# Optimization experiments

Measured on AMD Instinct MI355X. Metric: run time of the kernel, lower is better.

## Reference

```python
import jax, jax.numpy as jnp
import numpy as np

S, B, H = 2048, 4, 2048
NH = 16
HD = H // NH


def setup_inputs() -> dict:
    key = jax.random.key(0)
    ks = jax.random.split(key, 12)
    sc = 0.02
    return {
        "x": jax.random.normal(ks[0], (S, B, H), dtype=jnp.float32),
        "ln1_g": jnp.ones((H,), jnp.float32),
        "ln1_b": jnp.zeros((H,), jnp.float32),
        "qkv_w": jax.random.normal(ks[1], (3 * H, H), jnp.float32) * sc,
        "qkv_b": jnp.zeros((3 * H,), jnp.float32),
        "proj_w": jax.random.normal(ks[2], (H, H), jnp.float32) * sc,
        "proj_b": jnp.zeros((H,), jnp.float32),
        "ln2_g": jnp.ones((H,), jnp.float32),
        "ln2_b": jnp.zeros((H,), jnp.float32),
        "fc1_w": jax.random.normal(ks[3], (4 * H, H), jnp.float32) * sc,
        "fc1_b": jnp.zeros((4 * H,), jnp.float32),
        "fc2_w": jax.random.normal(ks[4], (H, 4 * H), jnp.float32) * sc,
        "fc2_b": jnp.zeros((H,), jnp.float32),
    }


def _layernorm(x, g, b, eps=1e-5):
    mu = jnp.mean(x, axis=-1, keepdims=True)
    var = jnp.mean((x - mu) ** 2, axis=-1, keepdims=True)
    return (x - mu) * jax.lax.rsqrt(var + eps) * g + b


def reference(x, ln1_g, ln1_b, qkv_w, qkv_b, proj_w, proj_b,
              ln2_g, ln2_b, fc1_w, fc1_b, fc2_w, fc2_b):
    # x: [S, B, H] (seq-first, as in original). Dropout is identity (eval mode).
    residual = x
    h = _layernorm(x, ln1_g, ln1_b)
    qkv = h @ qkv_w.T + qkv_b                       # [S, B, 3H]
    qkv = qkv.reshape(S, B, 3, NH, HD)
    q = jnp.transpose(qkv[:, :, 0], (1, 2, 0, 3))   # [B, NH, S, HD]
    k = jnp.transpose(qkv[:, :, 1], (1, 2, 0, 3))
    v = jnp.transpose(qkv[:, :, 2], (1, 2, 0, 3))
    scores = jnp.einsum("bhsd,bhtd->bhst", q, k) / jnp.sqrt(jnp.float32(HD))
    causal = jnp.tril(jnp.ones((S, S), dtype=bool))
    scores = jnp.where(causal, scores, jnp.float32(-jnp.inf))
    attn = jax.nn.softmax(scores, axis=-1)
    out = jnp.einsum("bhst,bhtd->bhsd", attn, v)    # [B, NH, S, HD]
    out = jnp.transpose(out, (2, 0, 1, 3)).reshape(S, B, H)
    out = out @ proj_w.T + proj_b
    x = residual + out
    residual = x
    h = _layernorm(x, ln2_g, ln2_b)
    h = h @ fc1_w.T + fc1_b
    h = jax.nn.gelu(h, approximate=False)
    h = h @ fc2_w.T + fc2_b
    return residual + h
```

## Files before the change

kernel.cpp:

```cpp
#include <hip/hip_runtime.h>
#include <hip/hip_bf16.h>
#include <cstdint>
#include <cstddef>

#define TOK 8192
#define HDIM 2048
#define H3 6144

typedef float f32x4 __attribute__((ext_vector_type(4)));
typedef short bf16x8 __attribute__((ext_vector_type(8)));
typedef int   i32x4 __attribute__((ext_vector_type(4)));
typedef unsigned short u16;
typedef unsigned int u32;
typedef u32 u32x2 __attribute__((ext_vector_type(2)));
typedef u32 u32x4 __attribute__((ext_vector_type(4)));

#define SLN  28.222222f
#define SW   1058.3333f
#define DQ   3.3480095e-5f

__device__ __forceinline__ u16 f2bf(float f) {
  union { float f; u32 u; } v; v.f = f;
  u32 u = v.u;
  return (u16)((u + 0x7fffu + ((u >> 16) & 1u)) >> 16);
}

__device__ __forceinline__ int q8(float v, float s) {
  int q = (int)rintf(v * s);
  return q < -127 ? -127 : (q > 127 ? 127 : q);
}

__device__ __forceinline__ float gelu_fast(float v) {
  const float u = 0.7978845608028654f * (v + 0.044715f * v * v * v);
  const float t = 1.0f - 2.0f / (__expf(2.0f * u) + 1.0f);
  return 0.5f * v * (1.0f + t);
}

__device__ __forceinline__ void gload16(const void* g, void* l) {
  __builtin_amdgcn_global_load_lds((const __attribute__((address_space(1))) u32*)g,
                                   (__attribute__((address_space(3))) u32*)l, 16, 0, 0);
}

#define GBAR()   __builtin_amdgcn_s_barrier()
#define GLGK0()  asm volatile("s_waitcnt lgkmcnt(0)" ::: "memory")
#define GVM(n)   asm volatile("s_waitcnt vmcnt(" #n ")" ::: "memory")
#define SCHED0() __builtin_amdgcn_sched_barrier(0)

__global__ __launch_bounds__(256)
void cvt_kernel(const float* __restrict__ in, u16* __restrict__ out, int n4) {
  int i = blockIdx.x * 256 + threadIdx.x;
  if (i >= n4) return;
  float4 v = ((const float4*)in)[i];
  union { u16 o[4]; u32x2 d; } t;
  t.o[0] = f2bf(v.x); t.o[1] = f2bf(v.y); t.o[2] = f2bf(v.z); t.o[3] = f2bf(v.w);
  ((u32x2*)out)[i] = t.d;
}

__global__ __launch_bounds__(256)
void cvt_i8_kernel(const float* __restrict__ in, char* __restrict__ out, int n4) {
  int i = blockIdx.x * 256 + threadIdx.x;
  if (i >= n4) return;
  float4 v = ((const float4*)in)[i];
  union { char c[4]; u32 d; } t;
  t.c[0] = (char)q8(v.x, SW); t.c[1] = (char)q8(v.y, SW);
  t.c[2] = (char)q8(v.z, SW); t.c[3] = (char)q8(v.w, SW);
  ((u32*)out)[i] = t.d;
}

template <int I8>
__global__ __launch_bounds__(256)
void ln_kernel(const float* __restrict__ x, const float* __restrict__ g,
               const float* __restrict__ bta, u16* __restrict__ out) {
  const int row = blockIdx.x, tid = threadIdx.x;
  const int lane = tid & 63, w = tid >> 6;
  const float* xr = x + (size_t)row * HDIM + tid * 8;
  float4 a = *(const float4*)xr;
  float4 c = *(const float4*)(xr + 4);
  float s = a.x + a.y + a.z + a.w + c.x + c.y + c.z + c.w;
  float q = a.x*a.x + a.y*a.y + a.z*a.z + a.w*a.w + c.x*c.x + c.y*c.y + c.z*c.z + c.w*c.w;
#pragma unroll
  for (int m = 32; m >= 1; m >>= 1) { s += __shfl_xor(s, m, 64); q += __shfl_xor(q, m, 64); }
  __shared__ float red[8];
  if (lane == 0) { red[w] = s; red[4 + w] = q; }
  __syncthreads();
  s = red[0] + red[1] + red[2] + red[3];
  q = red[4] + red[5] + red[6] + red[7];
  const float mu = s * (1.0f / HDIM);
  const float rstd = rsqrtf(q * (1.0f / HDIM) - mu * mu + 1e-5f);
  const float* gp = g + tid * 8; const float* bp = bta + tid * 8;
  float4 g0 = *(const float4*)gp, g1 = *(const float4*)(gp + 4);
  float4 b0 = *(const float4*)bp, b1 = *(const float4*)(bp + 4);
  float v[8];
  v[0] = (a.x - mu) * rstd * g0.x + b0.x;
  v[1] = (a.y - mu) * rstd * g0.y + b0.y;
  v[2] = (a.z - mu) * rstd * g0.z + b0.z;
  v[3] = (a.w - mu) * rstd * g0.w + b0.w;
  v[4] = (c.x - mu) * rstd * g1.x + b1.x;
  v[5] = (c.y - mu) * rstd * g1.y + b1.y;
  v[6] = (c.z - mu) * rstd * g1.z + b1.z;
  v[7] = (c.w - mu) * rstd * g1.w + b1.w;
  if constexpr (I8) {
    union { char c8[8]; u32x2 d; } t;
#pragma unroll
    for (int j = 0; j < 8; ++j) t.c8[j] = (char)q8(v[j], SLN);
    *(u32x2*)((char*)out + (size_t)row * HDIM + tid * 8) = t.d;
  } else {
    union { u16 o[8]; u32x4 d; } t;
#pragma unroll
    for (int j = 0; j < 8; ++j) t.o[j] = f2bf(v[j]);
    *(u32x4*)(out + (size_t)row * HDIM + tid * 8) = t.d;
  }
}

template <int EPI>
__global__ __launch_bounds__(256, 2)
void gemm128(const u16* __restrict__ A, const u16* __restrict__ Bm,
             const float* __restrict__ bias, const float* __restrict__ resid,
             u16* __restrict__ Cb, float* __restrict__ Cf, int M, int N, int K) {
  __shared__ u16 lds[16384];
  char* Lb = (char*)lds;
  const int tid = threadIdx.x;
  const int lane = tid & 63, w = tid >> 6;
  const int wr = w >> 1, wc = w & 1;
  const int l15 = lane & 15, hi = lane >> 4;

  const int tm = blockIdx.y * 128, tn = blockIdx.x * 128;

  const size_t rsK = (size_t)K * 2;
  const int scb = ((lane & 3) ^ ((lane >> 3) & 3)) * 16;
  const char* gA = (const char*)A + (size_t)(tm + w * 32 + (lane >> 2)) * rsK + scb;
  const char* gB = (const char*)Bm + (size_t)(tn + w * 32 + (lane >> 2)) * rsK + scb;
  char* sA = Lb + w * 2048;
  char* sB = Lb + 8192 + w * 2048;

#define STG(tt) do {                                                \
    const int _bo = ((tt) & 1) * 16384;                             \
    const size_t _ko = (size_t)(tt) * 64;                           \
    gload16(gA + _ko, sA + _bo);                                    \
    gload16(gA + _ko + (size_t)16 * rsK, sA + _bo + 1024);          \
    gload16(gB + _ko, sB + _bo);                                    \
    gload16(gB + _ko + (size_t)16 * rsK, sB + _bo + 1024);          \
  } while (0)

  f32x4 acc[4][4] = {};
  const int fo = (hi ^ ((l15 >> 1) & 3)) * 16;

  const int NT = K >> 5;
  STG(0);

  for (int t = 0; t < NT; ++t) {
    if (t + 1 < NT) { STG(t + 1); GVM(4); } else { GVM(0); }
    GBAR();

    const char* sb = Lb + (t & 1) * 16384;
    bf16x8 af[4], bfr[4];
#pragma unroll
    for (int i = 0; i < 4; ++i) {
      af[i]  = *(const bf16x8*)(sb + (wr * 64 + i * 16 + l15) * 64 + fo);
      bfr[i] = *(const bf16x8*)(sb + 8192 + (wc * 64 + i * 16 + l15) * 64 + fo);
    }
    __builtin_amdgcn_s_setprio(1);
#pragma unroll
    for (int mi = 0; mi < 4; ++mi)
#pragma unroll
      for (int ni = 0; ni < 4; ++ni)
        acc[mi][ni] = __builtin_amdgcn_mfma_f32_16x16x32_bf16(af[mi], bfr[ni], acc[mi][ni], 0, 0, 0);
    __builtin_amdgcn_s_setprio(0);
    GLGK0();
    GBAR();
  }

  const int colbase = tn + wc * 64 + l15;
  const int rowbase = tm + wr * 64 + hi * 4;
#pragma unroll
  for (int mi = 0; mi < 4; ++mi) {
#pragma unroll
    for (int ni = 0; ni < 4; ++ni) {
      const int col = colbase + ni * 16;
      const float bv = bias[col];
#pragma unroll
      for (int r = 0; r < 4; ++r) {
        const int row = rowbase + mi * 16 + r;
        float v = acc[mi][ni][r] + bv;
        if constexpr (EPI == 1) v = gelu_fast(v);
        const size_t idx = (size_t)row * N + col;
        if constexpr (EPI == 2) Cf[idx] = v + resid[idx];
        else                    Cb[idx] = f2bf(v);
      }
    }
  }
#undef STG
}

__global__ __launch_bounds__(256, 2)
void gemm128_i8(const char* __restrict__ A, const char* __restrict__ Bm,
                const float* __restrict__ bias, u16* __restrict__ Cb,
                int M, int N, int K) {
  __shared__ u16 lds[16384];
  char* Lb = (char*)lds;
  const int tid = threadIdx.x;
  const int lane = tid & 63, w = tid >> 6;
  const int wr = w >> 1, wc = w & 1;
  const int l15 = lane & 15, hi = lane >> 4;

  const int tm = blockIdx.y * 128, tn = blockIdx.x * 128;

  const size_t rsK = (size_t)K;
  const int scb = ((lane & 3) ^ ((lane >> 3) & 3)) * 16;
  const char* gA = A + (size_t)(tm + w * 32 + (lane >> 2)) * rsK + scb;
  const char* gB = Bm + (size_t)(tn + w * 32 + (lane >> 2)) * rsK + scb;
  char* sA = Lb + w * 2048;
  char* sB = Lb + 8192 + w * 2048;

#define STG(tt) do {                                                \
    const int _bo = ((tt) & 1) * 16384;                             \
    const size_t _ko = (size_t)(tt) * 64;                           \
    gload16(gA + _ko, sA + _bo);                                    \
    gload16(gA + _ko + (size_t)16 * rsK, sA + _bo + 1024);          \
    gload16(gB + _ko, sB + _bo);                                    \
    gload16(gB + _ko + (size_t)16 * rsK, sB + _bo + 1024);          \
  } while (0)

  i32x4 acc[4][4] = {};
  const int fo = (hi ^ ((l15 >> 1) & 3)) * 16;

  const int NT = K >> 6;
  STG(0);

  for (int t = 0; t < NT; ++t) {
    if (t + 1 < NT) { STG(t + 1); GVM(4); } else { GVM(0); }
    GBAR();

    const char* sb = Lb + (t & 1) * 16384;
    i32x4 af[4], bfr[4];
#pragma unroll
    for (int i = 0; i < 4; ++i) {
      af[i]  = *(const i32x4*)(sb + (wr * 64 + i * 16 + l15) * 64 + fo);
      bfr[i] = *(const i32x4*)(sb + 8192 + (wc * 64 + i * 16 + l15) * 64 + fo);
    }
    __builtin_amdgcn_s_setprio(1);
#pragma unroll
    for (int mi = 0; mi < 4; ++mi)
#pragma unroll
      for (int ni = 0; ni < 4; ++ni)
        acc[mi][ni] = __builtin_amdgcn_mfma_i32_16x16x64_i8(af[mi], bfr[ni], acc[mi][ni], 0, 0, 0);
    __builtin_amdgcn_s_setprio(0);
    GLGK0();
    GBAR();
  }

  const int colbase = tn + wc * 64 + l15;
  const int rowbase = tm + wr * 64 + hi * 4;
#pragma unroll
  for (int mi = 0; mi < 4; ++mi) {
#pragma unroll
    for (int ni = 0; ni < 4; ++ni) {
      const int col = colbase + ni * 16;
      const float bv = bias[col];
#pragma unroll
      for (int r = 0; r < 4; ++r) {
        const int row = rowbase + mi * 16 + r;
        float v = (float)acc[mi][ni][r] * DQ + bv;
        v = gelu_fast(v);
        Cb[(size_t)row * N + col] = f2bf(v);
      }
    }
  }
#undef STG
}

template <int EPI>
__global__ __launch_bounds__(512, 1)
void gemm256(const u16* __restrict__ A, const u16* __restrict__ Bm,
             const float* __restrict__ bias, const float* __restrict__ resid,
             u16* __restrict__ Cb, float* __restrict__ Cf, int M, int N, int K) {
  __shared__ u16 lds[65536];
  char* Lb = (char*)lds;
  const int tid = threadIdx.x;
  const int lane = tid & 63, w = tid >> 6;
  const int wm = w >> 2, wn = w & 3;
  const int l15 = lane & 15, hi = lane >> 4;

  const int gx = gridDim.x;
  const int nwg = gx * gridDim.y;
  int wgid = blockIdx.y * gx + blockIdx.x;
  wgid = (wgid & 7) * (nwg >> 3) + (wgid >> 3);
  const int tm = (wgid / gx) * 256, tn = (wgid % gx) * 256;

  const size_t rsK = (size_t)K * 2;
  const int srow8 = tid >> 3;
  const int scb   = ((tid & 7) ^ ((tid >> 3) & 7)) * 16;
  const char* gA = (const char*)A + (size_t)(tm + srow8) * rsK + scb;
  const char* gB = (const char*)Bm + (size_t)(tn + srow8) * rsK + scb;

#define STGH(o, h, tt) do {                                                    \
    char* _d = Lb + ((((tt) & 1) << 16) + (o) * 32768 + (h) * 16384 + tid * 16); \
    const char* _s = (o) ? gB : gA;                                            \
    const size_t _off = (size_t)(tt) * 128 + (size_t)((h) * 128) * rsK;        \
    gload16(_s + _off, _d);                                                    \
    gload16(_s + _off + (size_t)64 * rsK, _d + 8192);                          \
  } while (0)

  int koff[2];
#pragma unroll
  for (int ks = 0; ks < 2; ++ks) koff[ks] = ((ks * 4 + hi) ^ (l15 & 7)) * 16;

#define LDA(qm, dst) do {                                                      \
    _Pragma("unroll")                                                          \
    for (int mi4 = 0; mi4 < 4; ++mi4)                                          \
      _Pragma("unroll")                                                        \
      for (int ks = 0; ks < 2; ++ks)                                           \
        dst[mi4][ks] = *(const bf16x8*)(Lb + bb + wm * 16384 +                 \
            ((qm) * 64 + mi4 * 16 + l15) * 128 + koff[ks]);                    \
  } while (0)

#define LDB(qn) do {                                                           \
    _Pragma("unroll")                                                          \
    for (int ni = 0; ni < 2; ++ni)                                             \
      _Pragma("unroll")                                                        \
      for (int ks = 0; ks < 2; ++ks)                                           \
        bf[ni][ks] = *(const bf16x8*)(Lb + bb + 32768 + (wn >> 1) * 16384 +    \
            ((wn & 1) * 64 + (qn) * 32 + ni * 16 + l15) * 128 + koff[ks]);     \
  } while (0)

#define MFMA16(qm, qn, src) do {                                               \
    __builtin_amdgcn_s_setprio(1);                                             \
    _Pragma("unroll")                                                          \
    for (int ks = 0; ks < 2; ++ks)                                             \
      _Pragma("unroll")                                                        \
      for (int mi4 = 0; mi4 < 4; ++mi4)                                        \
        _Pragma("unroll")                                                      \
        for (int ni = 0; ni < 2; ++ni)                                         \
          acc[(qm) * 4 + mi4][(qn) * 2 + ni] =                                 \
            __builtin_amdgcn_mfma_f32_16x16x32_bf16(src[mi4][ks], bf[ni][ks],  \
                acc[(qm) * 4 + mi4][(qn) * 2 + ni], 0, 0, 0);                  \
    __builtin_amdgcn_s_setprio(0);                                             \
  } while (0)

  f32x4 acc[8][4] = {};
  bf16x8 af0[4][2], af1[4][2], bf[2][2];

  const int NT = K >> 6;

  STGH(0, 0, 0); STGH(0, 1, 0); STGH(1, 0, 0); STGH(1, 1, 0);
  STGH(0, 0, 1); STGH(0, 1, 1);
  SCHED0(); GVM(4); GBAR();

  for (int t = 0; t < NT; ++t) {
    const int bb = (t & 1) << 16;
    const bool sB = (t + 1 < NT), sA = (t + 2 < NT);
    LDA(0, af0); LDB(0);
    if (sB) STGH(1, 0, t + 1);
    SCHED0(); GBAR(); GLGK0(); SCHED0(); MFMA16(0, 0, af0); GBAR();
    LDA(1, af1);
    if (sB) STGH(1, 1, t + 1);
    SCHED0(); GBAR(); GLGK0(); SCHED0(); MFMA16(1, 0, af1); GBAR();
    LDB(1);
    if (sA) STGH(0, 0, t + 2);
    SCHED0(); GBAR(); GLGK0(); SCHED0(); MFMA16(0, 1, af0); GBAR();
    if (sA) STGH(0, 1, t + 2);
    SCHED0(); MFMA16(1, 1, af1);
    if (sA) GVM(4); else GVM(0);
    GBAR();
  }

#pragma unroll
  for (int mi = 0; mi < 8; ++mi) {
#pragma unroll
    for (int ni = 0; ni < 4; ++ni) {
      const int col = tn + wn * 64 + ni * 16 + l15;
      const float bv = bias[col];
#pragma unroll
      for (int r = 0; r < 4; ++r) {
        const int row = tm + wm * 128 + mi * 16 + hi * 4 + r;
        float v = acc[mi][ni][r] + bv;
        if constexpr (EPI == 1) v = gelu_fast(v);
        const size_t idx = (size_t)row * N + col;
        if constexpr (EPI == 2) Cf[idx] = v + resid[idx];
        else                    Cb[idx] = f2bf(v);
      }
    }
  }
#undef STGH
#undef LDA
#undef LDB
#undef MFMA16
}

__global__ __launch_bounds__(256)
void vtrans_kernel(const u16* __restrict__ qkv, u16* __restrict__ vt) {
  __shared__ u16 tile[32 * 136];
  const int s0 = blockIdx.x * 32;
  const int bh = blockIdx.y;
  const int b = bh >> 4, h = bh & 15;
  const int t = threadIdx.x;
  const int srow = t >> 3, scol = (t & 7) * 16;
  const u16* src = qkv + (size_t)((s0 + srow) * 4 + b) * H3 + 4096 + h * 128 + scol;
  *(bf16x8*)(tile + srow * 136 + scol)     = *(const bf16x8*)src;
  *(bf16x8*)(tile + srow * 136 + scol + 8) = *(const bf16x8*)(src + 8);
  __syncthreads();
  const int d = t >> 1, sc = (t & 1) * 16;
  union { u16 o[16]; u32x4 q[2]; } tmp;
#pragma unroll
  for (int i = 0; i < 16; ++i) tmp.o[i] = tile[(sc + i) * 136 + d];
  u16* dst = vt + ((size_t)bh * 128 + d) * 2048 + s0 + sc;
  *(u32x4*)dst       = tmp.q[0];
  *(u32x4*)(dst + 8) = tmp.q[1];
}

__global__ __launch_bounds__(256, 2)
void attn_kernel(const u16* __restrict__ qkv, const u16* __restrict__ vt,
                 u16* __restrict__ outb) {
  const int qt = 31 - blockIdx.x;
  const int bh = blockIdx.y;
  const int b = bh >> 4, h = bh & 15;
  const int tid = threadIdx.x, lane = tid & 63, w = tid >> 6;
  const int hi = lane >> 4, l15 = lane & 15;
  const int qs = qt * 64;

  __shared__ u16 Klds[64 * 128];
  __shared__ u16 Vlds[128 * 64];
  __shared__ u16 Plds[4 * 16 * 64];

  bf16x8 qf[4];
  {
    const int qrow = qs + w * 16 + l15;
    const u16* qp = qkv + (size_t)(qrow * 4 + b) * H3 + h * 128 + hi * 8;
#pragma unroll
    for (int kc = 0; kc < 4; ++kc) qf[kc] = *(const bf16x8*)(qp + kc * 32);
  }

  f32x4 o[8] = {};
  float mrun = -1e30f, lrun = 0.0f;

  const float sc = 0.08838834764831845f;
  char* plb = (char*)(Plds + w * 1024);

  const int krow = tid >> 2;
  const int kcb  = (tid & 3) * 64;
  const int vd   = tid >> 1;
  const int vhb  = (tid & 1) * 64;

  const int ntiles = qt + 1;
  for (int kt = 0; kt < ntiles; ++kt) {
    const int kv0 = kt * 64;
    const u16* ksrc = qkv + (size_t)((kv0 + krow) * 4 + b) * H3 + 2048 + h * 128 + kcb / 2;
    const u16* vsrc = vt + ((size_t)bh * 128 + vd) * 2048 + kv0 + (tid & 1) * 32;
    bf16x8 kr[4], vr[4];
#pragma unroll
    for (int c = 0; c < 4; ++c) { kr[c] = *(const bf16x8*)(ksrc + c * 8); vr[c] = *(const bf16x8*)(vsrc + c * 8); }

    __syncthreads();
#pragma unroll
    for (int c = 0; c < 4; ++c) {
      *(bf16x8*)((char*)Klds + ((krow * 256 + kcb + c * 16) ^ ((krow & 7) << 4))) = kr[c];
      *(bf16x8*)((char*)Vlds + ((vd * 128 + vhb + c * 16) ^ ((vd & 7) << 4)))     = vr[c];
    }
    __syncthreads();

    f32x4 s[4] = {};
#pragma unroll
    for (int kc = 0; kc < 4; ++kc) {
      const int dbyte = kc * 64 + hi * 16;
#pragma unroll
      for (int g = 0; g < 4; ++g) {
        const int row = g * 16 + l15;
        bf16x8 kf = *(const bf16x8*)((char*)Klds + ((row * 256 + dbyte) ^ ((l15 & 7) << 4)));
        s[g] = __builtin_amdgcn_mfma_f32_16x16x32_bf16(kf, qf[kc], s[g], 0, 0, 0);
      }
    }
#pragma unroll
    for (int g = 0; g < 4; ++g)
#pragma unroll
      for (int r = 0; r < 4; ++r) s[g][r] *= sc;

    if (kt == qt) {
      const int qrel = w * 16 + l15;
#pragma unroll
      for (int g = 0; g < 4; ++g)
#pragma unroll
        for (int r = 0; r < 4; ++r)
          if (g * 16 + hi * 4 + r > qrel) s[g][r] = -1e30f;
    }

    float pm = s[0][0];
#pragma unroll
    for (int g = 0; g < 4; ++g)
#pragma unroll
      for (int r = 0; r < 4; ++r) pm = fmaxf(pm, s[g][r]);
    pm = fmaxf(pm, __shfl_xor(pm, 16, 64));
    pm = fmaxf(pm, __shfl_xor(pm, 32, 64));

    const float mnew = fmaxf(mrun, pm);
    const bool need = mnew > mrun;
    const float corr = __expf(mrun - mnew);
    mrun = mnew;

    float p[4][4];
    float rs = 0.0f;
#pragma unroll
    for (int g = 0; g < 4; ++g)
#pragma unroll
      for (int r = 0; r < 4; ++r) { p[g][r] = __expf(s[g][r] - mnew); rs += p[g][r]; }
    rs += __shfl_xor(rs, 16, 64);
    rs += __shfl_xor(rs, 32, 64);
    lrun = lrun * corr + rs;

    if (__any(need)) {
      float corrq[4];
#pragma unroll
      for (int r = 0; r < 4; ++r) corrq[r] = __shfl(corr, hi * 4 + r, 64);
#pragma unroll
      for (int nf = 0; nf < 8; ++nf)
#pragma unroll
        for (int r = 0; r < 4; ++r) o[nf][r] *= corrq[r];
    }

#pragma unroll
    for (int g = 0; g < 4; ++g) {
      union { u16 h4[4]; u32x2 d; } pk;
#pragma unroll
      for (int r = 0; r < 4; ++r) pk.h4[r] = f2bf(p[g][r]);
      *(u32x2*)(plb + ((l15 * 128 + g * 32 + hi * 8) ^ ((l15 & 7) << 4))) = pk.d;
    }
    asm volatile("s_waitcnt lgkmcnt(0)" ::: "memory");
    bf16x8 pf[2];
#pragma unroll
    for (int hk = 0; hk < 2; ++hk)
      pf[hk] = *(const bf16x8*)(plb + ((l15 * 128 + hk * 64 + hi * 16) ^ ((l15 & 7) << 4)));

#pragma unroll
    for (int hk = 0; hk < 2; ++hk)
#pragma unroll
      for (int nf = 0; nf < 8; ++nf) {
        bf16x8 vf = *(const bf16x8*)((char*)Vlds +
                      (((nf * 16 + l15) * 128 + hk * 64 + hi * 16) ^ ((l15 & 7) << 4)));
        o[nf] = __builtin_amdgcn_mfma_f32_16x16x32_bf16(pf[hk], vf, o[nf], 0, 0, 0);
      }
  }

  const float inv = 1.0f / lrun;
  float invq[4];
#pragma unroll
  for (int r = 0; r < 4; ++r) invq[r] = __shfl(inv, hi * 4 + r, 64);
#pragma unroll
  for (int nf = 0; nf < 8; ++nf) {
#pragma unroll
    for (int r = 0; r < 4; ++r) {
      const int rl = hi * 4 + r;
      const int t = (qs + w * 16 + rl) * 4 + b;
      outb[(size_t)t * HDIM + h * 128 + nf * 16 + l15] = f2bf(o[nf][r] * invq[r]);
    }
  }
}

extern "C" void kernel_launch(void* const* d_in, const int* in_sizes, int n_in,
                              void* d_out, int out_size, void* d_ws, size_t ws_size,
                              hipStream_t stream) {
  const float* x     = (const float*)d_in[0];
  const float* ln1g  = (const float*)d_in[1];
  const float* ln1b  = (const float*)d_in[2];
  const float* qkvw  = (const float*)d_in[3];
  const float* qkvb  = (const float*)d_in[4];
  const float* projw = (const float*)d_in[5];
  const float* projb = (const float*)d_in[6];
  const float* ln2g  = (const float*)d_in[7];
  const float* ln2b  = (const float*)d_in[8];
  const float* fc1w  = (const float*)d_in[9];
  const float* fc1b  = (const float*)d_in[10];
  const float* fc2w  = (const float*)d_in[11];
  const float* fc2b  = (const float*)d_in[12];
  float* out = (float*)d_out;

  u16* wbuf = (u16*)d_ws;
  u16* pbuf = (u16*)((char*)d_ws + (size_t)32 * 1024 * 1024);
  u16* qbuf = (u16*)((char*)d_ws + (size_t)64 * 1024 * 1024);
  u16* vtg  = (u16*)d_ws;
  u16* aout = (u16*)((char*)d_ws + (size_t)160 * 1024 * 1024);

  dim3 blk(256);
  dim3 gblk(512);

  ln_kernel<0><<<8192, blk, 0, stream>>>(x, ln1g, ln1b, pbuf);
  cvt_kernel<<<12288, blk, 0, stream>>>(qkvw, wbuf, 3145728);
  gemm256<0><<<dim3(24, 32), gblk, 0, stream>>>(pbuf, wbuf, qkvb, nullptr, qbuf, nullptr, 8192, 6144, 2048);
  vtrans_kernel<<<dim3(64, 64), blk, 0, stream>>>(qbuf, vtg);
  attn_kernel<<<dim3(32, 64), blk, 0, stream>>>(qbuf, vtg, aout);
  cvt_kernel<<<4096, blk, 0, stream>>>(projw, wbuf, 1048576);
  gemm128<2><<<dim3(16, 64), blk, 0, stream>>>(aout, wbuf, projb, x, nullptr, out, 8192, 2048, 2048);
  ln_kernel<1><<<8192, blk, 0, stream>>>(out, ln2g, ln2b, pbuf);
  cvt_i8_kernel<<<16384, blk, 0, stream>>>(fc1w, (char*)wbuf, 4194304);
  gemm128_i8<<<dim3(64, 64), blk, 0, stream>>>((const char*)pbuf, (const char*)wbuf, fc1b, qbuf, 8192, 8192, 2048);
  cvt_kernel<<<16384, blk, 0, stream>>>(fc2w, wbuf, 4194304);
  gemm256<2><<<dim3(8, 32), gblk, 0, stream>>>(qbuf, wbuf, fc2b, out, nullptr, out, 8192, 2048, 8192);
}
```

Before: 1.033 ms.

## Double-buffer K/V tiles in LDS with two-ahead register prefetch in attention

The attention kernel now keeps two LDS buffers for K and V. It prefetches tile kt+2 into registers while computing tile kt, and writes tile kt+1 into the other buffer during the current tile's QK phase. This replaces two barriers per tile with one and overlaps global loads with MFMA and softmax work. The cost is twice the K/V LDS footprint (about 72KB per block with launch_bounds 256,2) and extra register pressure from holding two prefetch register sets, either of which may reduce occupancy or cause spills.

```diff
diff --git a/kernel.cpp b/kernel.cpp
--- a/kernel.cpp
+++ b/kernel.cpp
@@ -418,8 +418,8 @@
   const int hi = lane >> 4, l15 = lane & 15;
   const int qs = qt * 64;
 
-  __shared__ u16 Klds[64 * 128];
-  __shared__ u16 Vlds[128 * 64];
+  __shared__ u16 Klds[2][64 * 128];
+  __shared__ u16 Vlds[2][128 * 64];
   __shared__ u16 Plds[4 * 16 * 64];
 
   bf16x8 qf[4];
@@ -434,7 +434,7 @@
   float mrun = -1e30f, lrun = 0.0f;
 
   const float sc = 0.08838834764831845f;
-  char* plb = (char*)(Plds + w * 1024);
+  char* plb = (char*)Plds + w * 2048;
 
   const int krow = tid >> 2;
   const int kcb  = (tid & 3) * 64;
@@ -442,102 +442,120 @@
   const int vhb  = (tid & 1) * 64;
 
   const int ntiles = qt + 1;
-  for (int kt = 0; kt < ntiles; ++kt) {
-    const int kv0 = kt * 64;
-    const u16* ksrc = qkv + (size_t)((kv0 + krow) * 4 + b) * H3 + 2048 + h * 128 + kcb / 2;
-    const u16* vsrc = vt + ((size_t)bh * 128 + vd) * 2048 + kv0 + (tid & 1) * 32;
-    bf16x8 kr[4], vr[4];
-#pragma unroll
-    for (int c = 0; c < 4; ++c) { kr[c] = *(const bf16x8*)(ksrc + c * 8); vr[c] = *(const bf16x8*)(vsrc + c * 8); }
-
-    __syncthreads();
-#pragma unroll
-    for (int c = 0; c < 4; ++c) {
-      *(bf16x8*)((char*)Klds + ((krow * 256 + kcb + c * 16) ^ ((krow & 7) << 4))) = kr[c];
-      *(bf16x8*)((char*)Vlds + ((vd * 128 + vhb + c * 16) ^ ((vd & 7) << 4)))     = vr[c];
-    }
-    __syncthreads();
-
-    f32x4 s[4] = {};
-#pragma unroll
-    for (int kc = 0; kc < 4; ++kc) {
-      const int dbyte = kc * 64 + hi * 16;
-#pragma unroll
-      for (int g = 0; g < 4; ++g) {
-        const int row = g * 16 + l15;
-        bf16x8 kf = *(const bf16x8*)((char*)Klds + ((row * 256 + dbyte) ^ ((l15 & 7) << 4)));
-        s[g] = __builtin_amdgcn_mfma_f32_16x16x32_bf16(kf, qf[kc], s[g], 0, 0, 0);
-      }
-    }
-#pragma unroll
-    for (int g = 0; g < 4; ++g)
-#pragma unroll
-      for (int r = 0; r < 4; ++r) s[g][r] *= sc;
-
-    if (kt == qt) {
-      const int qrel = w * 16 + l15;
-#pragma unroll
-      for (int g = 0; g < 4; ++g)
-#pragma unroll
-        for (int r = 0; r < 4; ++r)
-          if (g * 16 + hi * 4 + r > qrel) s[g][r] = -1e30f;
-    }
-
-    float pm = s[0][0];
-#pragma unroll
-    for (int g = 0; g < 4; ++g)
-#pragma unroll
-      for (int r = 0; r < 4; ++r) pm = fmaxf(pm, s[g][r]);
-    pm = fmaxf(pm, __shfl_xor(pm, 16, 64));
-    pm = fmaxf(pm, __shfl_xor(pm, 32, 64));
-
-    const float mnew = fmaxf(mrun, pm);
-    const bool need = mnew > mrun;
-    const float corr = __expf(mrun - mnew);
-    mrun = mnew;
-
-    float p[4][4];
-    float rs = 0.0f;
-#pragma unroll
-    for (int g = 0; g < 4; ++g)
-#pragma unroll
-      for (int r = 0; r < 4; ++r) { p[g][r] = __expf(s[g][r] - mnew); rs += p[g][r]; }
-    rs += __shfl_xor(rs, 16, 64);
-    rs += __shfl_xor(rs, 32, 64);
-    lrun = lrun * corr + rs;
-
-    if (__any(need)) {
-      float corrq[4];
-#pragma unroll
-      for (int r = 0; r < 4; ++r) corrq[r] = __shfl(corr, hi * 4 + r, 64);
-#pragma unroll
-      for (int nf = 0; nf < 8; ++nf)
-#pragma unroll
-        for (int r = 0; r < 4; ++r) o[nf][r] *= corrq[r];
-    }
-
-#pragma unroll
-    for (int g = 0; g < 4; ++g) {
-      union { u16 h4[4]; u32x2 d; } pk;
-#pragma unroll
-      for (int r = 0; r < 4; ++r) pk.h4[r] = f2bf(p[g][r]);
-      *(u32x2*)(plb + ((l15 * 128 + g * 32 + hi * 8) ^ ((l15 & 7) << 4))) = pk.d;
-    }
-    asm volatile("s_waitcnt lgkmcnt(0)" ::: "memory");
-    bf16x8 pf[2];
-#pragma unroll
-    for (int hk = 0; hk < 2; ++hk)
-      pf[hk] = *(const bf16x8*)(plb + ((l15 * 128 + hk * 64 + hi * 16) ^ ((l15 & 7) << 4)));
-
-#pragma unroll
-    for (int hk = 0; hk < 2; ++hk)
-#pragma unroll
-      for (int nf = 0; nf < 8; ++nf) {
-        bf16x8 vf = *(const bf16x8*)((char*)Vlds +
-                      (((nf * 16 + l15) * 128 + hk * 64 + hi * 16) ^ ((l15 & 7) << 4)));
-        o[nf] = __builtin_amdgcn_mfma_f32_16x16x32_bf16(pf[hk], vf, o[nf], 0, 0, 0);
-      }
-  }
+
+  bf16x8 krA[4], vrA[4], krB[4], vrB[4];
+
+#define LOADT(tt, kr, vr) do {                                                  \
+    const u16* ks_ = qkv + (size_t)(((tt) * 64 + krow) * 4 + b) * H3 + 2048 + h * 128 + kcb / 2; \
+    const u16* vs_ = vt + ((size_t)bh * 128 + vd) * 2048 + (tt) * 64 + (tid & 1) * 32; \
+    _Pragma("unroll")                                                           \
+    for (int c = 0; c < 4; ++c) { kr[c] = *(const bf16x8*)(ks_ + c * 8);        \
+                                  vr[c] = *(const bf16x8*)(vs_ + c * 8); }      \
+  } while (0)
+
+#define WRITET(bb, kr, vr) do {                                                 \
+    _Pragma("unroll")                                                           \
+    for (int c = 0; c < 4; ++c) {                                               \
+      *(bf16x8*)((char*)Klds[bb] + ((krow * 256 + kcb + c * 16) ^ ((krow & 7) << 4))) = kr[c]; \
+      *(bf16x8*)((char*)Vlds[bb] + ((vd * 128 + vhb + c * 16) ^ ((vd & 7) << 4)))     = vr[c]; \
+    }                                                                           \
+  } while (0)
+
+#define TILE_BODY(CUR, KRN, VRN, KRL, VRL) do {                                 \
+              \
+    f32x4 s[4] = {};                                                            \
+    _Pragma("unroll")                                                           \
+    for (int kc = 0; kc < 4; ++kc) {                                            \
+      const int dbyte = kc * 64 + hi * 16;                                      \
+      _Pragma("unroll")                                                         \
+      for (int g = 0; g < 4; ++g) {                                             \
+        const int row = g * 16 + l15;                                           \
+        bf16x8 kf = *(const bf16x8*)((char*)Klds[CUR] + ((row * 256 + dbyte) ^ ((l15 & 7) << 4))); \
+        s[g] = __builtin_amdgcn_mfma_f32_16x16x32_bf16(kf, qf[kc], s[g], 0, 0, 0); \
+      }                                                                         \
+    }                                                                           \
+    \
+    if (kt + 1 < ntiles) WRITET(CUR ^ 1, KRN, VRN);                             \
+    if (kt + 2 < ntiles) LOADT(kt + 2, KRL, VRL);                               \
+    _Pragma("unroll")                                                           \
+    for (int g = 0; g < 4; ++g)                                                 \
+      _Pragma("unroll")                                                         \
+      for (int r = 0; r < 4; ++r) s[g][r] *= sc;                                \
+    if (kt == qt) {                                                             \
+      const int qrel = w * 16 + l15;                                            \
+      _Pragma("unroll")                                                         \
+      for (int g = 0; g < 4; ++g)                                               \
+        _Pragma("unroll")                                                       \
+        for (int r = 0; r < 4; ++r)                                             \
+          if (g * 16 + hi * 4 + r > qrel) s[g][r] = -1e30f;                     \
+    }                                                                           \
+    float pm = s[0][0];                                                         \
+    _Pragma("unroll")                                                           \
+    for (int g = 0; g < 4; ++g)                                                 \
+      _Pragma("unroll")                                                         \
+      for (int r = 0; r < 4; ++r) pm = fmaxf(pm, s[g][r]);                      \
+    pm = fmaxf(pm, __shfl_xor(pm, 16, 64));                                     \
+    pm = fmaxf(pm, __shfl_xor(pm, 32, 64));                                     \
+    const float mnew = fmaxf(mrun, pm);                                         \
+    const bool need = mnew > mrun;                                              \
+    const float corr = __expf(mrun - mnew);                                     \
+    mrun = mnew;                                                                \
+    float p[4][4];                                                              \
+    float rs = 0.0f;                                                            \
+    _Pragma("unroll")                                                           \
+    for (int g = 0; g < 4; ++g)                                                 \
+      _Pragma("unroll")                                                         \
+      for (int r = 0; r < 4; ++r) { p[g][r] = __expf(s[g][r] - mnew); rs += p[g][r]; } \
+    rs += __shfl_xor(rs, 16, 64);                                               \
+    rs += __shfl_xor(rs, 32, 64);                                               \
+    lrun = lrun * corr + rs;                                                    \
+    if (__any(need)) {                                                          \
+      float corrq[4];                                                           \
+      _Pragma("unroll")                                                         \
+      for (int r = 0; r < 4; ++r) corrq[r] = __shfl(corr, hi * 4 + r, 64);      \
+      _Pragma("unroll")                                                         \
+      for (int nf = 0; nf < 8; ++nf)                                            \
+        _Pragma("unroll")                                                       \
+        for (int r = 0; r < 4; ++r) o[nf][r] *= corrq[r];                       \
+    }                                                                           \
+    _Pragma("unroll")                                                           \
+    for (int g = 0; g < 4; ++g) {                                               \
+      union { u16 h4[4]; u32x2 d; } pk;                                         \
+      _Pragma("unroll")                                                         \
+      for (int r = 0; r < 4; ++r) pk.h4[r] = f2bf(p[g][r]);                     \
+      *(u32x2*)(plb + ((l15 * 128 + g * 32 + hi * 8) ^ ((l15 & 7) << 4))) = pk.d; \
+    }                                                                           \
+    asm volatile("s_waitcnt lgkmcnt(0)" ::: "memory");                          \
+    bf16x8 pf[2];                                                               \
+    _Pragma("unroll")                                                           \
+    for (int hk = 0; hk < 2; ++hk)                                              \
+      pf[hk] = *(const bf16x8*)(plb + ((l15 * 128 + hk * 64 + hi * 16) ^ ((l15 & 7) << 4))); \
+    _Pragma("unroll")                                                           \
+    for (int hk = 0; hk < 2; ++hk)                                              \
+      _Pragma("unroll")                                                         \
+      for (int nf = 0; nf < 8; ++nf) {                                          \
+        bf16x8 vf = *(const bf16x8*)((char*)Vlds[CUR] +                         \
+                      (((nf * 16 + l15) * 128 + hk * 64 + hi * 16) ^ ((l15 & 7) << 4))); \
+        o[nf] = __builtin_amdgcn_mfma_f32_16x16x32_bf16(pf[hk], vf, o[nf], 0, 0, 0); \
+      }                                                                         \
+    __syncthreads();                                                            \
+  } while (0)
+
+  LOADT(0, krA, vrA);
+  if (ntiles > 1) LOADT(1, krB, vrB);
+  WRITET(0, krA, vrA);
+  __syncthreads();
+
+  int kt = 0;
+  while (true) {
+    TILE_BODY(0, krB, vrB, krA, vrA);
+    ++kt; if (kt >= ntiles) break;
+    TILE_BODY(1, krA, vrA, krB, vrB);
+    ++kt; if (kt >= ntiles) break;
+  }
+#undef LOADT
+#undef WRITET
+#undef TILE_BODY
 
   const float inv = 1.0f / lrun;
   float invq[4];
```

Result: slower. 1.059 ms (+2.4%).
